# Optimization experiments

Measured on AMD Instinct MI355X. Metric: run time of the kernel, lower is better.

## Reference

```python
import jax, jax.numpy as jnp
import numpy as np

NUM_HEADS = 8
EPS = 1e-6


def conv1x1(x, w, b):
    # x: [b,c,h,w], w: [out,in], b: [out]  (torch Conv2d 1x1 weight squeezed)
    return jnp.einsum('bchw,oc->bohw', x, w) + b[None, :, None, None]


def feature_map(x):
    return jax.nn.elu(x) + 1.0


def setup_inputs() -> dict:
    key = jax.random.key(0)
    ks = jax.random.split(key, 9)
    C = 512
    s = 1.0 / np.sqrt(C)
    x = jax.random.normal(ks[0], (8, C, 64, 64), dtype=jnp.float32)
    wq = jax.random.normal(ks[1], (C, C), dtype=jnp.float32) * s
    wk = jax.random.normal(ks[2], (C, C), dtype=jnp.float32) * s
    wv = jax.random.normal(ks[3], (C, C), dtype=jnp.float32) * s
    wo = jax.random.normal(ks[4], (C, C), dtype=jnp.float32) * s
    bq = jax.random.normal(ks[5], (C,), dtype=jnp.float32) * 0.01
    bk = jax.random.normal(ks[6], (C,), dtype=jnp.float32) * 0.01
    bv = jax.random.normal(ks[7], (C,), dtype=jnp.float32) * 0.01
    bo = jax.random.normal(ks[8], (C,), dtype=jnp.float32) * 0.01
    return {'x': x, 'wq': wq, 'bq': bq, 'wk': wk, 'bk': bk,
            'wv': wv, 'bv': bv, 'wo': wo, 'bo': bo}


def reference(x, wq, bq, wk, bk, wv, bv, wo, bo):
    b, c, h, w = x.shape
    nh = NUM_HEADS
    hd = c // nh
    L = h * w

    def to_heads(t):
        # [b,c,h,w] -> [b,nh,L,hd]
        return t.reshape(b, nh, hd, L).transpose(0, 1, 3, 2)

    Q = feature_map(to_heads(conv1x1(x, wq, bq)))
    K = feature_map(to_heads(conv1x1(x, wk, bk)))
    V = to_heads(conv1x1(x, wv, bv)) / L  # values / v_length

    KV = jnp.einsum('bhld,bhlv->bhdv', K, V)                 # [b,nh,hd,hd]
    Z = 1.0 / (jnp.einsum('bhld,bhd->bhl', Q, K.sum(axis=-2)) + EPS)
    out = jnp.einsum('bhld,bhdv,bhl->bhlv', Q, KV, Z) * L    # [b,nh,L,hd]

    out = out.transpose(0, 1, 3, 2).reshape(b, c, h, w)
    return conv1x1(out, wo, bo)
```

## Files before the change

kernel.cpp:

```cpp
#include <hip/hip_runtime.h>
#include <hip/hip_bf16.h>
#include <stdint.h>

#define BATCH 8
#define CCH   512
#define NHD   8
#define HD    64
#define LLEN  4096
#define M1    1536

typedef __bf16 bf16x8 __attribute__((ext_vector_type(8)));
typedef __bf16 bf16x4 __attribute__((ext_vector_type(4)));
typedef float  f32x4  __attribute__((ext_vector_type(4)));

__device__ __forceinline__ f32x4 mfma16(bf16x8 a, bf16x8 b, f32x4 c) {
  return __builtin_amdgcn_mfma_f32_16x16x32_bf16(a, b, c, 0, 0, 0);
}

__device__ __forceinline__ void gload_lds16(const void* g, void* l) {
  __builtin_amdgcn_global_load_lds(
      (const __attribute__((address_space(1))) uint32_t*)(uintptr_t)g,
      (__attribute__((address_space(3))) uint32_t*)(uintptr_t)l,
      16, 0, 0);
}

__global__ void pack_w(const float* __restrict__ wq, const float* __restrict__ wk,
                       const float* __restrict__ wv, const float* __restrict__ wo,
                       const float* __restrict__ bq, const float* __restrict__ bk,
                       const float* __restrict__ bv,
                       __bf16* __restrict__ wqkvb, __bf16* __restrict__ wob,
                       float* __restrict__ biasq) {
  const int n = M1 * CCH + CCH * CCH + M1;
  for (int i = blockIdx.x * blockDim.x + threadIdx.x; i < n; i += gridDim.x * blockDim.x) {
    if (i < M1 * CCH) {
      int r = i >> 9, c = i & 511;
      float v = (r < 512) ? wq[r * 512 + c]
              : (r < 1024) ? wk[(r - 512) * 512 + c]
                           : wv[(r - 1024) * 512 + c];
      wqkvb[i] = (__bf16)v;
    } else if (i < M1 * CCH + CCH * CCH) {
      int j = i - M1 * CCH;
      wob[j] = (__bf16)wo[j];
    } else {
      int j = i - M1 * CCH - CCH * CCH;
      biasq[j] = (j < 512) ? bq[j] : (j < 1024) ? bk[j - 512] : bv[j - 1024];
    }
  }
}

__global__ __launch_bounds__(256) void transpose_x(const float* __restrict__ x,
                                                   __bf16* __restrict__ xt) {
  __shared__ float tile[64][65];
  const int b = blockIdx.z, c0 = blockIdx.y * 64, l0 = blockIdx.x * 64;
  const int t = threadIdx.x;
  const int lq = (t & 15) * 4, cr = t >> 4;
  const float* xp = x + ((size_t)b * CCH + c0) * LLEN + l0;
#pragma unroll
  for (int q = 0; q < 4; ++q) {
    const int c = cr + q * 16;
    float4 v = *(const float4*)(xp + (size_t)c * LLEN + lq);
    tile[c][lq + 0] = v.x;
    tile[c][lq + 1] = v.y;
    tile[c][lq + 2] = v.z;
    tile[c][lq + 3] = v.w;
  }
  __syncthreads();
  __bf16* xo = xt + ((size_t)b * LLEN + l0) * CCH + c0;
  const int c4 = (t & 15) * 4, lr = t >> 4;
#pragma unroll
  for (int p = 0; p < 4; ++p) {
    const int l = lr + p * 16;
    bf16x4 o;
#pragma unroll
    for (int i = 0; i < 4; ++i) o[i] = (__bf16)tile[c4 + i][l];
    *(bf16x4*)(xo + (size_t)l * CCH + c4) = o;
  }
}

#define STAGE_A(kt, base)                                                    \
  {                                                                          \
    _Pragma("unroll") for (int p = 0; p < 2; ++p)                            \
        gload_lds16(Ag + (size_t)sR[p] * CCH + (kt) * 32 + sK[p],            \
                    lds + (base) + sDst[p]);                                 \
  }
#define STAGE_B(kt, base)                                                    \
  {                                                                          \
    _Pragma("unroll") for (int p = 0; p < 2; ++p)                            \
        gload_lds16(Bg + (size_t)sR[p] * CCH + (kt) * 32 + sK[p],            \
                    lds + (base) + 8192 + sDst[p]);                          \
  }

template <int EPI>
__global__ __launch_bounds__(512, 2) void gemm256(
    const __bf16* __restrict__ A, const __bf16* __restrict__ Bm,
    const float* __restrict__ bias,
    __bf16* __restrict__ qt, __bf16* __restrict__ kcm, __bf16* __restrict__ vcm,
    float* __restrict__ out) {
  __shared__ __attribute__((aligned(16))) __bf16 lds[3 * 16384];
  const int b  = blockIdx.z;
  const int n0 = blockIdx.x * 256;
  const int m0 = blockIdx.y * 256;
  const int tid = threadIdx.x;
  const int ll = tid & 63, w = tid >> 6;
  const int wr = w >> 2, wc = w & 3;
  const int lhi = ll >> 4, llo = ll & 15;

  int aoff[8], boff[4];
#pragma unroll
  for (int m = 0; m < 8; ++m) {
    int R = wr * 128 + m * 16 + llo;
    aoff[m] = ((R >> 1) << 6) + (((((R & 1) << 2) | lhi) ^ ((R >> 1) & 7)) << 3);
  }
#pragma unroll
  for (int n = 0; n < 4; ++n) {
    int R = wc * 64 + n * 16 + llo;
    boff[n] = ((R >> 1) << 6) + (((((R & 1) << 2) | lhi) ^ ((R >> 1) & 7)) << 3) + 8192;
  }

  int sR[2], sK[2], sDst[2];
#pragma unroll
  for (int p = 0; p < 2; ++p) {
    int idx = p * 512 + tid;
    int r2 = idx >> 3, c7u = (idx & 7) ^ (r2 & 7);
    sR[p]   = (r2 << 1) | (c7u >> 2);
    sK[p]   = (c7u & 3) << 3;
    sDst[p] = idx * 8;
  }
  const __bf16* Ag = A + (size_t)m0 * CCH;
  const __bf16* Bg = Bm + ((size_t)b * LLEN + n0) * CCH;

  STAGE_A(0, 0) STAGE_B(0, 0)
  STAGE_A(1, 16384) STAGE_B(1, 16384)
  asm volatile("s_waitcnt vmcnt(4)" ::: "memory");
  __builtin_amdgcn_s_barrier();

  f32x4 acc[8][4] = {};
  int bi = 0;
  for (int t = 0; t < 16; ++t) {
    const int abase = bi * 16384;
    const int sb = ((bi == 0) ? 2 : bi - 1) * 16384;
    bf16x8 af[4], bfr[4];
#pragma unroll
    for (int i = 0; i < 4; ++i) af[i] = *(const bf16x8*)(lds + abase + aoff[i]);
#pragma unroll
    for (int j = 0; j < 4; ++j) bfr[j] = *(const bf16x8*)(lds + abase + boff[j]);
    if (t + 2 < 16) STAGE_A(t + 2, sb)
    __builtin_amdgcn_s_barrier();
    asm volatile("s_waitcnt lgkmcnt(0)" ::: "memory");
    __builtin_amdgcn_sched_barrier(0);
    __builtin_amdgcn_s_setprio(1);
#pragma unroll
    for (int i = 0; i < 4; ++i)
#pragma unroll
      for (int j = 0; j < 4; ++j) acc[i][j] = mfma16(af[i], bfr[j], acc[i][j]);
    __builtin_amdgcn_s_setprio(0);
    __builtin_amdgcn_s_barrier();
#pragma unroll
    for (int i = 0; i < 4; ++i) af[i] = *(const bf16x8*)(lds + abase + aoff[4 + i]);
    if (t + 2 < 16) {
      STAGE_B(t + 2, sb)
      asm volatile("s_waitcnt vmcnt(4)" ::: "memory");
    } else {
      asm volatile("s_waitcnt vmcnt(0)" ::: "memory");
    }
    __builtin_amdgcn_s_barrier();
    asm volatile("s_waitcnt lgkmcnt(0)" ::: "memory");
    __builtin_amdgcn_sched_barrier(0);
    __builtin_amdgcn_s_setprio(1);
#pragma unroll
    for (int i = 0; i < 4; ++i)
#pragma unroll
      for (int j = 0; j < 4; ++j) acc[4 + i][j] = mfma16(af[i], bfr[j], acc[4 + i][j]);
    __builtin_amdgcn_s_setprio(0);
    __builtin_amdgcn_s_barrier();
    bi = (bi == 2) ? 0 : bi + 1;
  }

#pragma unroll
  for (int i = 0; i < 8; ++i) {
    const int o0 = m0 + wr * 128 + i * 16 + lhi * 4;
#pragma unroll
    for (int j = 0; j < 4; ++j) {
      const int col = n0 + wc * 64 + j * 16 + llo;
      if (EPI == 0) {
        if (m0 < 512) {
          bf16x4 pk;
#pragma unroll
          for (int r = 0; r < 4; ++r) {
            float tv = acc[i][j][r] + bias[o0 + r];
            tv = tv > 0.f ? tv + 1.f : __expf(tv);
            pk[r] = (__bf16)tv;
          }
          *(bf16x4*)(qt + ((size_t)b * LLEN + col) * CCH + o0) = pk;
        } else if (m0 < 1024) {
#pragma unroll
          for (int r = 0; r < 4; ++r) {
            float tv = acc[i][j][r] + bias[o0 + r];
            tv = tv > 0.f ? tv + 1.f : __expf(tv);
            kcm[((size_t)b * CCH + (o0 - 512 + r)) * LLEN + col] = (__bf16)tv;
          }
        } else {
#pragma unroll
          for (int r = 0; r < 4; ++r)
            vcm[((size_t)b * CCH + (o0 - 1024 + r)) * LLEN + col] =
                (__bf16)(acc[i][j][r] + bias[o0 + r]);
        }
      } else {
#pragma unroll
        for (int r = 0; r < 4; ++r)
          out[((size_t)b * CCH + o0 + r) * LLEN + col] = acc[i][j][r] + bias[o0 + r];
      }
    }
  }
}

__global__ __launch_bounds__(64) void kv_part_k(const __bf16* __restrict__ kcm,
                                                const __bf16* __restrict__ vcm,
                                                float* __restrict__ part,
                                                float* __restrict__ part_ks) {
  const int lc = blockIdx.x, bh = blockIdx.y;
  const int b = bh >> 3, h = bh & 7;
  const int ll = threadIdx.x, lhi = ll >> 4, llo = ll & 15;
  const __bf16* Kp = kcm + ((size_t)b * CCH + h * 64) * LLEN;
  const __bf16* Vp = vcm + ((size_t)b * CCH + h * 64) * LLEN;
  f32x4 acc[4][4];
#pragma unroll
  for (int i = 0; i < 4; ++i)
#pragma unroll
    for (int j = 0; j < 4; ++j) acc[i][j] = (f32x4){0.f, 0.f, 0.f, 0.f};
  float ks[4] = {0.f, 0.f, 0.f, 0.f};
  const int base = lc * 512 + lhi * 8;
  for (int kt = 0; kt < 16; ++kt) {
    const int k0 = base + kt * 32;
    bf16x8 af[4], bfr[4];
#pragma unroll
    for (int i = 0; i < 4; ++i) af[i]  = *(const bf16x8*)(Kp + (size_t)(i * 16 + llo) * LLEN + k0);
#pragma unroll
    for (int i = 0; i < 4; ++i) bfr[i] = *(const bf16x8*)(Vp + (size_t)(i * 16 + llo) * LLEN + k0);
#pragma unroll
    for (int i = 0; i < 4; ++i)
#pragma unroll
      for (int r = 0; r < 8; ++r) ks[i] += (float)af[i][r];
#pragma unroll
    for (int i = 0; i < 4; ++i)
#pragma unroll
      for (int j = 0; j < 4; ++j) acc[i][j] = mfma16(af[i], bfr[j], acc[i][j]);
  }
  float* op = part + ((size_t)lc * 64 + bh) * 4096;
#pragma unroll
  for (int i = 0; i < 4; ++i)
#pragma unroll
    for (int j = 0; j < 4; ++j)
#pragma unroll
      for (int r = 0; r < 4; ++r) {
        int d = i * 16 + lhi * 4 + r, v = j * 16 + llo;
        op[d * 64 + v] = acc[i][j][r];
      }
  float* pks = part_ks + ((size_t)lc * 64 + bh) * 64;
#pragma unroll
  for (int i = 0; i < 4; ++i) {
    float s = ks[i];
    s += __shfl_xor(s, 16);
    s += __shfl_xor(s, 32);
    if (lhi == 0) pks[i * 16 + llo] = s;
  }
}

__global__ void kv_red_k(const float* __restrict__ part, float* __restrict__ kv) {
  const int i = blockIdx.x * blockDim.x + threadIdx.x;
  float s = 0.f;
#pragma unroll
  for (int lc = 0; lc < 8; ++lc) s += part[(size_t)lc * 262144 + i];
  kv[i] = s;
}

__global__ void ksum_red_k(const float* __restrict__ part_ks, float* __restrict__ ksum) {
  const int i = blockIdx.x * blockDim.x + threadIdx.x;
  float s = 0.f;
#pragma unroll
  for (int lc = 0; lc < 8; ++lc) s += part_ks[(size_t)lc * 4096 + i];
  ksum[i] = s;
}

__global__ __launch_bounds__(256) void apply_k(const __bf16* __restrict__ qt,
                                               const float* __restrict__ kv,
                                               const float* __restrict__ ksum,
                                               __bf16* __restrict__ attn) {
  __shared__ __attribute__((aligned(16))) __bf16 kvT[64 * 68];
  __shared__ float zb[256];
  const int lc = blockIdx.x, bh = blockIdx.y;
  const int b = bh >> 3, h = bh & 7;
  const int tid = threadIdx.x;
  const float* kvp = kv + (size_t)bh * 4096;
  for (int i = tid; i < 4096; i += 256) {
    int d = i >> 6, v = i & 63;
    kvT[v * 68 + d] = (__bf16)kvp[i];
  }
  const int l = lc * 256 + tid;
  const __bf16* qp = qt + ((size_t)b * LLEN + l) * CCH + h * 64;
  const float* ksp = ksum + bh * 64;
  float s = 0.f;
#pragma unroll
  for (int d8 = 0; d8 < 64; d8 += 8) {
    bf16x8 qv = *(const bf16x8*)(qp + d8);
#pragma unroll
    for (int i = 0; i < 8; ++i) s += (float)qv[i] * ksp[d8 + i];
  }
  zb[tid] = 1.0f / (s + 1e-6f);
  __syncthreads();

  const int ll = tid & 63, w = tid >> 6, lhi = ll >> 4, llo = ll & 15;
  f32x4 acc[4][4];
#pragma unroll
  for (int i = 0; i < 4; ++i)
#pragma unroll
    for (int j = 0; j < 4; ++j) acc[i][j] = (f32x4){0.f, 0.f, 0.f, 0.f};
  const __bf16* qbase = qt + ((size_t)b * LLEN + lc * 256 + w * 64) * CCH + h * 64;
#pragma unroll
  for (int kt = 0; kt < 2; ++kt) {
    const int k8 = kt * 32 + lhi * 8;
    bf16x8 af[4], bfr[4];
#pragma unroll
    for (int i = 0; i < 4; ++i)
      af[i] = *(const bf16x8*)(qbase + (size_t)(i * 16 + llo) * CCH + k8);
#pragma unroll
    for (int j = 0; j < 4; ++j) {
      const __bf16* pb = kvT + (j * 16 + llo) * 68 + k8;
      ((bf16x4*)&bfr[j])[0] = *(const bf16x4*)pb;
      ((bf16x4*)&bfr[j])[1] = *(const bf16x4*)(pb + 4);
    }
#pragma unroll
    for (int i = 0; i < 4; ++i)
#pragma unroll
      for (int j = 0; j < 4; ++j) acc[i][j] = mfma16(af[i], bfr[j], acc[i][j]);
  }
  __bf16* ap = attn + ((size_t)b * LLEN + lc * 256) * CCH + h * 64;
#pragma unroll
  for (int i = 0; i < 4; ++i)
#pragma unroll
    for (int j = 0; j < 4; ++j)
#pragma unroll
      for (int r = 0; r < 4; ++r) {
        int ml = w * 64 + i * 16 + lhi * 4 + r;
        int v = j * 16 + llo;
        ap[(size_t)ml * CCH + v] = (__bf16)(acc[i][j][r] * zb[ml]);
      }
}

extern "C" void kernel_launch(void* const* d_in, const int* in_sizes, int n_in,
                              void* d_out, int out_size, void* d_ws, size_t ws_size,
                              hipStream_t stream) {
  const float* x  = (const float*)d_in[0];
  const float* wq = (const float*)d_in[1];
  const float* bq = (const float*)d_in[2];
  const float* wk = (const float*)d_in[3];
  const float* bk = (const float*)d_in[4];
  const float* wv = (const float*)d_in[5];
  const float* bv = (const float*)d_in[6];
  const float* wo = (const float*)d_in[7];
  const float* bo = (const float*)d_in[8];
  float* out = (float*)d_out;

  char* p = (char*)d_ws;
  __bf16* xt    = (__bf16*)p; p += (size_t)BATCH * LLEN * CCH * 2;
  __bf16* qt    = (__bf16*)p; p += (size_t)BATCH * LLEN * CCH * 2;
  __bf16* kcm   = (__bf16*)p; p += (size_t)BATCH * CCH * LLEN * 2;
  __bf16* vcm   = (__bf16*)p; p += (size_t)BATCH * CCH * LLEN * 2;
  __bf16* wqkvb = (__bf16*)p; p += (size_t)M1 * CCH * 2;
  __bf16* wob   = (__bf16*)p; p += (size_t)CCH * CCH * 2;
  float*  biasq = (float*)p;  p += (size_t)M1 * 4;
  float*  ksum  = (float*)p;  p += (size_t)BATCH * CCH * 4;
  float*  part  = (float*)p;  p += (size_t)8 * 64 * HD * HD * 4;
  float*  kvb   = (float*)p;  p += (size_t)64 * HD * HD * 4;
  float*  pks   = (float*)p;  p += (size_t)8 * 64 * 64 * 4;
  __bf16* attn  = xt;

  pack_w<<<1024, 256, 0, stream>>>(wq, wk, wv, wo, bq, bk, bv, wqkvb, wob, biasq);
  transpose_x<<<dim3(64, 8, BATCH), 256, 0, stream>>>(x, xt);
  gemm256<0><<<dim3(16, 6, BATCH), 512, 0, stream>>>(wqkvb, xt, biasq, qt, kcm, vcm, nullptr);
  kv_part_k<<<dim3(8, 64), 64, 0, stream>>>(kcm, vcm, part, pks);
  kv_red_k<<<1024, 256, 0, stream>>>(part, kvb);
  ksum_red_k<<<16, 256, 0, stream>>>(pks, ksum);
  apply_k<<<dim3(16, 64), 256, 0, stream>>>(qt, kvb, ksum, attn);
  gemm256<1><<<dim3(16, 2, BATCH), 512, 0, stream>>>(wob, attn, bo, nullptr, nullptr, nullptr, out);
}
```

Before: 170.2 us.

## Restructure GEMM main loop with register double-buffered LDS reads; widen kv_part

```diff
diff --git a/kernel.cpp b/kernel.cpp
--- a/kernel.cpp
+++ b/kernel.cpp
@@ -77,17 +77,23 @@
   }
 }
 
-#define STAGE_A(kt, base)                                                    \
+#define STAGE4(tt)                                                           \
   {                                                                          \
-    _Pragma("unroll") for (int p = 0; p < 2; ++p)                            \
-        gload_lds16(Ag + (size_t)sR[p] * CCH + (kt) * 32 + sK[p],            \
-                    lds + (base) + sDst[p]);                                 \
-  }
-#define STAGE_B(kt, base)                                                    \
+    const int tK = (tt) * 32;                                                \
+    const int bs = ((tt) % 3) * 16384;                                       \
+    gload_lds16(Ag + sOff + tK,         lds + bs + tid * 8);                 \
+    gload_lds16(Ag + sOff + 65536 + tK, lds + bs + 4096 + tid * 8);          \
+    gload_lds16(Bg + sOff + tK,         lds + bs + 8192 + tid * 8);          \
+    gload_lds16(Bg + sOff + 65536 + tK, lds + bs + 12288 + tid * 8);         \
+  }
+#define READS12(tt)                                                          \
   {                                                                          \
-    _Pragma("unroll") for (int p = 0; p < 2; ++p)                            \
-        gload_lds16(Bg + (size_t)sR[p] * CCH + (kt) * 32 + sK[p],            \
-                    lds + (base) + 8192 + sDst[p]);                          \
+    const int rb = ((tt) % 3) * 16384;                                       \
+    const int s = (tt) & 1;                                                  \
+    _Pragma("unroll") for (int m = 0; m < 8; ++m)                            \
+        aS[s][m] = *(const bf16x8*)(lds + rb + aLane + m * 512);             \
+    _Pragma("unroll") for (int n = 0; n < 4; ++n)                            \
+        bS[s][n] = *(const bf16x8*)(lds + rb + bLane + n * 512);             \
   }
 
 template <int EPI>
@@ -105,75 +111,47 @@
   const int wr = w >> 2, wc = w & 3;
   const int lhi = ll >> 4, llo = ll & 15;
 
-  int aoff[8], boff[4];
-#pragma unroll
-  for (int m = 0; m < 8; ++m) {
-    int R = wr * 128 + m * 16 + llo;
-    aoff[m] = ((R >> 1) << 6) + (((((R & 1) << 2) | lhi) ^ ((R >> 1) & 7)) << 3);
-  }
-#pragma unroll
-  for (int n = 0; n < 4; ++n) {
-    int R = wc * 64 + n * 16 + llo;
-    boff[n] = ((R >> 1) << 6) + (((((R & 1) << 2) | lhi) ^ ((R >> 1) & 7)) << 3) + 8192;
-  }
-
-  int sR[2], sK[2], sDst[2];
-#pragma unroll
-  for (int p = 0; p < 2; ++p) {
-    int idx = p * 512 + tid;
-    int r2 = idx >> 3, c7u = (idx & 7) ^ (r2 & 7);
-    sR[p]   = (r2 << 1) | (c7u >> 2);
-    sK[p]   = (c7u & 3) << 3;
-    sDst[p] = idx * 8;
-  }
+  const int Ra = wr * 128 + llo;
+  const int aLane = ((Ra >> 1) << 6) + (((((Ra & 1) << 2) | lhi) ^ ((Ra >> 1) & 7)) << 3);
+  const int Rb = wc * 64 + llo;
+  const int bLane = 8192 + ((Rb >> 1) << 6) + (((((Rb & 1) << 2) | lhi) ^ ((Rb >> 1) & 7)) << 3);
+
+  const int r2s = tid >> 3, c7u = (tid & 7) ^ (r2s & 7);
+  const int sRow = (r2s << 1) | (c7u >> 2);
+  const int sOff = sRow * CCH + ((c7u & 3) << 3);
+
   const __bf16* Ag = A + (size_t)m0 * CCH;
   const __bf16* Bg = Bm + ((size_t)b * LLEN + n0) * CCH;
 
-  STAGE_A(0, 0) STAGE_B(0, 0)
-  STAGE_A(1, 16384) STAGE_B(1, 16384)
+  bf16x8 aS[2][8], bS[2][4];
+  f32x4 acc[8][4] = {};
+
+  STAGE4(0)
+  STAGE4(1)
   asm volatile("s_waitcnt vmcnt(4)" ::: "memory");
-  __builtin_amdgcn_s_barrier();
-
-  f32x4 acc[8][4] = {};
-  int bi = 0;
+  asm volatile("s_barrier" ::: "memory");
+  READS12(0)
+
+#pragma unroll
   for (int t = 0; t < 16; ++t) {
-    const int abase = bi * 16384;
-    const int sb = ((bi == 0) ? 2 : bi - 1) * 16384;
-    bf16x8 af[4], bfr[4];
-#pragma unroll
-    for (int i = 0; i < 4; ++i) af[i] = *(const bf16x8*)(lds + abase + aoff[i]);
-#pragma unroll
-    for (int j = 0; j < 4; ++j) bfr[j] = *(const bf16x8*)(lds + abase + boff[j]);
-    if (t + 2 < 16) STAGE_A(t + 2, sb)
-    __builtin_amdgcn_s_barrier();
-    asm volatile("s_waitcnt lgkmcnt(0)" ::: "memory");
+    asm volatile("s_barrier" ::: "memory");
+    if (t < 14) STAGE4(t + 2)
+    if (t < 14) asm volatile("s_waitcnt vmcnt(4)" ::: "memory");
+    else        asm volatile("s_waitcnt vmcnt(0)" ::: "memory");
+    asm volatile("s_barrier" ::: "memory");
+    if (t < 15) READS12(t + 1)
+    if (t < 15) asm volatile("s_waitcnt lgkmcnt(12)" ::: "memory");
+    else        asm volatile("s_waitcnt lgkmcnt(0)" ::: "memory");
     __builtin_amdgcn_sched_barrier(0);
     __builtin_amdgcn_s_setprio(1);
-#pragma unroll
-    for (int i = 0; i < 4; ++i)
-#pragma unroll
-      for (int j = 0; j < 4; ++j) acc[i][j] = mfma16(af[i], bfr[j], acc[i][j]);
+    {
+      const int s = t & 1;
+#pragma unroll
+      for (int m = 0; m < 8; ++m)
+#pragma unroll
+        for (int n = 0; n < 4; ++n) acc[m][n] = mfma16(aS[s][m], bS[s][n], acc[m][n]);
+    }
     __builtin_amdgcn_s_setprio(0);
-    __builtin_amdgcn_s_barrier();
-#pragma unroll
-    for (int i = 0; i < 4; ++i) af[i] = *(const bf16x8*)(lds + abase + aoff[4 + i]);
-    if (t + 2 < 16) {
-      STAGE_B(t + 2, sb)
-      asm volatile("s_waitcnt vmcnt(4)" ::: "memory");
-    } else {
-      asm volatile("s_waitcnt vmcnt(0)" ::: "memory");
-    }
-    __builtin_amdgcn_s_barrier();
-    asm volatile("s_waitcnt lgkmcnt(0)" ::: "memory");
-    __builtin_amdgcn_sched_barrier(0);
-    __builtin_amdgcn_s_setprio(1);
-#pragma unroll
-    for (int i = 0; i < 4; ++i)
-#pragma unroll
-      for (int j = 0; j < 4; ++j) acc[4 + i][j] = mfma16(af[i], bfr[j], acc[4 + i][j]);
-    __builtin_amdgcn_s_setprio(0);
-    __builtin_amdgcn_s_barrier();
-    bi = (bi == 2) ? 0 : bi + 1;
   }
 
 #pragma unroll
@@ -214,13 +192,16 @@
   }
 }
 
-__global__ __launch_bounds__(64) void kv_part_k(const __bf16* __restrict__ kcm,
-                                                const __bf16* __restrict__ vcm,
-                                                float* __restrict__ part,
-                                                float* __restrict__ part_ks) {
+__global__ __launch_bounds__(256) void kv_part_k(const __bf16* __restrict__ kcm,
+                                                 const __bf16* __restrict__ vcm,
+                                                 float* __restrict__ part,
+                                                 float* __restrict__ part_ks) {
+  __shared__ float red[8192];
+  __shared__ float ksred[4][64];
   const int lc = blockIdx.x, bh = blockIdx.y;
   const int b = bh >> 3, h = bh & 7;
-  const int ll = threadIdx.x, lhi = ll >> 4, llo = ll & 15;
+  const int tid = threadIdx.x;
+  const int w = tid >> 6, ll = tid & 63, lhi = ll >> 4, llo = ll & 15;
   const __bf16* Kp = kcm + ((size_t)b * CCH + h * 64) * LLEN;
   const __bf16* Vp = vcm + ((size_t)b * CCH + h * 64) * LLEN;
   f32x4 acc[4][4];
@@ -229,8 +210,9 @@
 #pragma unroll
     for (int j = 0; j < 4; ++j) acc[i][j] = (f32x4){0.f, 0.f, 0.f, 0.f};
   float ks[4] = {0.f, 0.f, 0.f, 0.f};
-  const int base = lc * 512 + lhi * 8;
-  for (int kt = 0; kt < 16; ++kt) {
+  const int base = lc * 512 + w * 128 + lhi * 8;
+#pragma unroll
+  for (int kt = 0; kt < 4; ++kt) {
     const int k0 = base + kt * 32;
     bf16x8 af[4], bfr[4];
 #pragma unroll
@@ -246,23 +228,53 @@
 #pragma unroll
       for (int j = 0; j < 4; ++j) acc[i][j] = mfma16(af[i], bfr[j], acc[i][j]);
   }
-  float* op = part + ((size_t)lc * 64 + bh) * 4096;
-#pragma unroll
-  for (int i = 0; i < 4; ++i)
-#pragma unroll
-    for (int j = 0; j < 4; ++j)
-#pragma unroll
-      for (int r = 0; r < 4; ++r) {
-        int d = i * 16 + lhi * 4 + r, v = j * 16 + llo;
-        op[d * 64 + v] = acc[i][j][r];
-      }
-  float* pks = part_ks + ((size_t)lc * 64 + bh) * 64;
 #pragma unroll
   for (int i = 0; i < 4; ++i) {
     float s = ks[i];
     s += __shfl_xor(s, 16);
     s += __shfl_xor(s, 32);
-    if (lhi == 0) pks[i * 16 + llo] = s;
+    if (lhi == 0) ksred[w][i * 16 + llo] = s;
+  }
+  if (w >= 2) {
+#pragma unroll
+    for (int i = 0; i < 4; ++i)
+#pragma unroll
+      for (int j = 0; j < 4; ++j)
+        *(f32x4*)(red + (((w - 2) * 16 + i * 4 + j) << 8) + ll * 4) = acc[i][j];
+  }
+  __syncthreads();
+  if (w < 2) {
+#pragma unroll
+    for (int i = 0; i < 4; ++i)
+#pragma unroll
+      for (int j = 0; j < 4; ++j)
+        acc[i][j] += *(const f32x4*)(red + ((w * 16 + i * 4 + j) << 8) + ll * 4);
+  }
+  float ksv = 0.f;
+  if (w == 1) ksv = ksred[0][ll] + ksred[1][ll] + ksred[2][ll] + ksred[3][ll];
+  __syncthreads();
+  if (w == 1) {
+#pragma unroll
+    for (int i = 0; i < 4; ++i)
+#pragma unroll
+      for (int j = 0; j < 4; ++j)
+        *(f32x4*)(red + ((i * 4 + j) << 8) + ll * 4) = acc[i][j];
+    part_ks[((size_t)lc * 64 + bh) * 64 + ll] = ksv;
+  }
+  __syncthreads();
+  if (w == 0) {
+    float* op = part + ((size_t)lc * 64 + bh) * 4096;
+#pragma unroll
+    for (int i = 0; i < 4; ++i)
+#pragma unroll
+      for (int j = 0; j < 4; ++j) {
+        acc[i][j] += *(const f32x4*)(red + ((i * 4 + j) << 8) + ll * 4);
+#pragma unroll
+        for (int r = 0; r < 4; ++r) {
+          int d = i * 16 + lhi * 4 + r, v = j * 16 + llo;
+          op[d * 64 + v] = acc[i][j][r];
+        }
+      }
   }
 }
 
@@ -378,7 +390,7 @@
   pack_w<<<1024, 256, 0, stream>>>(wq, wk, wv, wo, bq, bk, bv, wqkvb, wob, biasq);
   transpose_x<<<dim3(64, 8, BATCH), 256, 0, stream>>>(x, xt);
   gemm256<0><<<dim3(16, 6, BATCH), 512, 0, stream>>>(wqkvb, xt, biasq, qt, kcm, vcm, nullptr);
-  kv_part_k<<<dim3(8, 64), 64, 0, stream>>>(kcm, vcm, part, pks);
+  kv_part_k<<<dim3(8, 64), 256, 0, stream>>>(kcm, vcm, part, pks);
   kv_red_k<<<1024, 256, 0, stream>>>(part, kvb);
   ksum_red_k<<<16, 256, 0, stream>>>(pks, ksum);
   apply_k<<<dim3(16, 64), 256, 0, stream>>>(qt, kvb, ksum, attn);
```

New measurement: 170.2 us. No clear change (-0.0%).
